# Kernel tuning notes

Hardware: AMD Instinct MI355X
Metric: run time of the kernel (lower is better)

## Reference

```python
import jax, jax.numpy as jnp
import numpy as np

WS = 8          # window_size
DISP = WS // 2  # cyclic shift displacement
HEADS = 12
HEAD_DIM = 32
SCALE = HEAD_DIM ** -0.5


def _rel_indices():
    # indices of (x, y) for x in range(WS) for y in range(WS)
    idx = np.stack(np.meshgrid(np.arange(WS), np.arange(WS), indexing='ij'), -1).reshape(-1, 2)
    return idx[None, :, :] - idx[:, None, :] + WS - 1  # (WS^2, WS^2, 2), values in [0, 2*WS-2]


def _masks():
    ninf = -np.inf
    # upper/lower mask: blocks attention across the vertical wrap boundary
    m_ul = np.zeros((WS * WS, WS * WS), np.float32)
    m_ul[-DISP * WS:, :-DISP * WS] = ninf
    m_ul[:-DISP * WS, -DISP * WS:] = ninf
    # left/right mask: blocks attention across the horizontal wrap boundary
    m4 = np.zeros((WS, WS, WS, WS), np.float32)  # (h1, w1, h2, w2)
    m4[:, -DISP:, :, :-DISP] = ninf
    m4[:, :-DISP, :, -DISP:] = ninf
    m_lr = m4.reshape(WS * WS, WS * WS)
    return jnp.asarray(m_ul), jnp.asarray(m_lr)


def setup_inputs() -> dict:
    key = jax.random.key(0)
    k1, k2, k3, k4, k5 = jax.random.split(key, 5)
    dim = HEADS * HEAD_DIM  # 384
    return {
        'x': jax.random.normal(k1, (16, 64, 64, dim), jnp.float32),
        'w_qkv': jax.random.normal(k2, (dim, 3 * dim), jnp.float32) * 0.02,
        'pos_embedding': jax.random.normal(k3, (2 * WS - 1, 2 * WS - 1), jnp.float32),
        'w_out': jax.random.normal(k4, (dim, dim), jnp.float32) * 0.02,
        'b_out': jax.random.normal(k5, (dim,), jnp.float32) * 0.02,
    }


def reference(x, w_qkv, pos_embedding, w_out, b_out):
    b, H, W, dim = x.shape
    nw_h, nw_w = H // WS, W // WS
    # cyclic shift
    x = jnp.roll(x, (-DISP, -DISP), axis=(1, 2))
    qkv = x @ w_qkv  # (b, H, W, 3*inner)

    def to_windows(t):
        # (b, H, W, inner) -> (b, heads, nw_h*nw_w, WS*WS, head_dim)
        t = t.reshape(b, nw_h, WS, nw_w, WS, HEADS, HEAD_DIM)
        return t.transpose(0, 5, 1, 3, 2, 4, 6).reshape(b, HEADS, nw_h * nw_w, WS * WS, HEAD_DIM)

    q, k, v = [to_windows(t) for t in jnp.split(qkv, 3, axis=-1)]
    dots = jnp.einsum('bhwid,bhwjd->bhwij', q, k) * SCALE

    rel = _rel_indices()
    dots = dots + pos_embedding[rel[..., 0], rel[..., 1]]  # relative position bias

    m_ul, m_lr = _masks()
    dots = dots.at[:, :, -nw_w:].add(m_ul)            # last row of windows
    dots = dots.at[:, :, nw_w - 1::nw_w].add(m_lr)    # last column of windows

    attn = jax.nn.softmax(dots, axis=-1)
    out = jnp.einsum('bhwij,bhwjd->bhwid', attn, v)
    # windows -> image layout
    out = out.reshape(b, HEADS, nw_h, nw_w, WS, WS, HEAD_DIM)
    out = out.transpose(0, 2, 4, 3, 5, 1, 6).reshape(b, H, W, HEADS * HEAD_DIM)
    out = out @ w_out + b_out
    # cyclic back shift
    return jnp.roll(out, (DISP, DISP), axis=(1, 2))
```

## Files before the change

kernel.cpp:

```cpp
#include <hip/hip_runtime.h>
#include <stdint.h>

#define HEADS 12
#define HD 32
#define DIM 384
#define NQKV 1152
#define NPIX 4096
#define NB 16

typedef __attribute__((ext_vector_type(8))) short bf16x8;
typedef __attribute__((ext_vector_type(4))) short bf16x4;
typedef __attribute__((ext_vector_type(4))) float f32x4;

__device__ __forceinline__ unsigned short f2bf(float f) {
  uint32_t u = __builtin_bit_cast(uint32_t, f);
  u += 0x7FFF + ((u >> 16) & 1);
  return (unsigned short)(u >> 16);
}

#define GL_LDS(gp, lp) __builtin_amdgcn_global_load_lds( \
    (const __attribute__((address_space(1))) void*)(gp),  \
    (__attribute__((address_space(3))) void*)(lp), 16, 0, 0)

__global__ void convert_all(const float* __restrict__ x,
                            const float* __restrict__ wqkv,
                            const float* __restrict__ wout,
                            const float* __restrict__ pos,
                            unsigned short* __restrict__ xb,
                            unsigned short* __restrict__ wqkvT,
                            unsigned short* __restrict__ woutT,
                            float* __restrict__ tab) {
  int bid = blockIdx.x;
  if (bid < 12288) {
    int i = bid * 256 + threadIdx.x;
    const float4* xp = (const float4*)x;
    float4 a = xp[2 * i], b2 = xp[2 * i + 1];
    union { bf16x8 v; unsigned short s[8]; } u;
    u.s[0] = f2bf(a.x);  u.s[1] = f2bf(a.y);
    u.s[2] = f2bf(a.z);  u.s[3] = f2bf(a.w);
    u.s[4] = f2bf(b2.x); u.s[5] = f2bf(b2.y);
    u.s[6] = f2bf(b2.z); u.s[7] = f2bf(b2.w);
    ((bf16x8*)xb)[i] = u.v;
  } else if (bid < 14016) {
    int tid = (bid - 12288) * 256 + threadIdx.x;
    if (tid < NQKV * DIM) {
      int n = tid / DIM, k = tid % DIM;
      wqkvT[tid] = f2bf(wqkv[(size_t)k * NQKV + n]);
    }
    if (tid < DIM * DIM) {
      int n = tid / DIM, k = tid % DIM;
      woutT[tid] = f2bf(wout[(size_t)k * DIM + n]);
    }
  } else {
    int tid = (bid - 14016) * 256 + threadIdx.x;
    int v = tid >> 12, rem = tid & 4095;
    int i = rem >> 6, j = rem & 63;
    int xi = i >> 3, yi = i & 7, xj = j >> 3, yj = j & 7;
    float val = pos[(xj - xi + 7) * 15 + (yj - yi + 7)];
    if ((v & 1) && ((i >= 32) != (j >= 32))) val = -1e30f;
    if ((v & 2) && ((yi >= 4) != (yj >= 4))) val = -1e30f;
    tab[tid] = val;
  }
}

__global__ __launch_bounds__(256, 4) void gemm_qkv(
    const unsigned short* __restrict__ xb,
    const unsigned short* __restrict__ wT,
    unsigned short* __restrict__ qkv)
{
  __shared__ unsigned short lA[128 * 64];
  __shared__ unsigned short lB[128 * 64];
  const int tid = threadIdx.x;
  const int wid = tid >> 6, lane = tid & 63;
  const int wr = wid >> 1, wc = wid & 1;
  const int lr = lane >> 4, lc = lane & 15;

  const int f = blockIdx.x;
  const int xcd = f & 7, idx = f >> 3;
  const int nt = idx % 9, mt = xcd * 64 + idx / 9;
  const int m0 = mt * 128, n0 = nt * 128;

  const int srow = wid * 32 + (lane >> 3);
  const int scol = ((lane & 7) ^ (lane >> 3)) * 8;
  const unsigned short* agp = xb + (size_t)(m0 + srow) * DIM + scol;
  const unsigned short* bgp = wT + (size_t)(n0 + srow) * DIM + scol;

  const f32x4 z4 = {0.f, 0.f, 0.f, 0.f};
  f32x4 acc[4][4];
#pragma unroll
  for (int i = 0; i < 4; i++)
#pragma unroll
    for (int j = 0; j < 4; j++) acc[i][j] = z4;

  auto stage = [&](int t) {
#pragma unroll
    for (int i = 0; i < 4; i++) {
      GL_LDS(agp + (size_t)(i * 8) * DIM + t * 64, &lA[(wid * 4 + i) * 512]);
      GL_LDS(bgp + (size_t)(i * 8) * DIM + t * 64, &lB[(wid * 4 + i) * 512]);
    }
  };
  auto compute = [&]() {
    const int sw = lc & 7;
#pragma unroll
    for (int kk = 0; kk < 2; kk++) {
      bf16x8 afr[4], bfr[4];
#pragma unroll
      for (int mi = 0; mi < 4; mi++)
        afr[mi] = *(const bf16x8*)&lA[(wr * 64 + mi * 16 + lc) * 64 + (((kk * 4 + lr) ^ sw) * 8)];
#pragma unroll
      for (int ni = 0; ni < 4; ni++)
        bfr[ni] = *(const bf16x8*)&lB[(wc * 64 + ni * 16 + lc) * 64 + (((kk * 4 + lr) ^ sw) * 8)];
#pragma unroll
      for (int mi = 0; mi < 4; mi++)
#pragma unroll
        for (int ni = 0; ni < 4; ni++)
          acc[mi][ni] = __builtin_amdgcn_mfma_f32_16x16x32_bf16(afr[mi], bfr[ni], acc[mi][ni], 0, 0, 0);
    }
  };

  for (int t = 0; t < 6; ++t) {
    stage(t);
    __syncthreads();
    compute();
    if (t < 5) __syncthreads();
  }

#pragma unroll
  for (int mi = 0; mi < 4; mi++) {
    int row = m0 + wr * 64 + mi * 16 + lr * 4;
#pragma unroll
    for (int reg = 0; reg < 4; reg++) {
      size_t rb = (size_t)(row + reg) * NQKV + n0 + wc * 64 + lc;
#pragma unroll
      for (int ni = 0; ni < 4; ni++)
        qkv[rb + ni * 16] = f2bf(acc[mi][ni][reg]);
    }
  }
}

__global__ __launch_bounds__(256) void attn_kernel(
    const unsigned short* __restrict__ qkv,
    const float* __restrict__ tab,
    unsigned short* __restrict__ Z)
{
  __shared__ unsigned short Vt[4][32 * 80];

  const int wid = threadIdx.x >> 6, lane = threadIdx.x & 63;
  const int lr = lane >> 4, lc = lane & 15;
  const int task = blockIdx.x * 4 + wid;
  const int win = task & 63;
  const int head = (task >> 6) % HEADS;
  const int b = task / (HEADS * 64);
  const int wh = win >> 3, ww = win & 7;
  const float* tv = tab + (((wh == 7) ? 1 : 0) + ((ww == 7) ? 2 : 0)) * 4096;

  auto pixof = [&](int t) {
    int hh = (wh * 8 + (t >> 3) + 4) & 63;
    int w2 = (ww * 8 + (t & 7) + 4) & 63;
    return hh * 64 + w2;
  };

  unsigned short* vt = &Vt[wid][0];
  bf16x8 qf[4], kf[4];
#pragma unroll
  for (int g = 0; g < 4; ++g) {
    int t = g * 16 + lc;
    const unsigned short* base =
        qkv + (size_t)(b * NPIX + pixof(t)) * NQKV + head * HD + lr * 8;
    qf[g] = *(const bf16x8*)(base);
    kf[g] = *(const bf16x8*)(base + DIM);
    union { bf16x8 v; unsigned short s[8]; } uv;
    uv.v = *(const bf16x8*)(base + 2 * DIM);
#pragma unroll
    for (int j = 0; j < 8; j++) {
      int row = lr * 8 + j;
      int addr = row * 80 + (((g * 2 + (lc >> 3)) ^ ((row >> 2) & 3)) << 3) + (lc & 7);
      vt[addr] = uv.s[j];
    }
  }

  const float SC = 0.17677669529663687f;
  const f32x4 z4 = {0.f, 0.f, 0.f, 0.f};
  uint32_t pf[4][2][4];
  const int srcA = (lc + 16 * (2 * (lr & 1))) << 2;
  const int srcB = srcA + 64;
  const bool hiSel = (lr >> 1) != 0;

#pragma unroll
  for (int bq = 0; bq < 4; bq++) {
    f32x4 tb[4];
#pragma unroll
    for (int a = 0; a < 4; a++)
      tb[a] = *(const f32x4*)&tv[(bq * 16 + lc) * 64 + a * 16 + lr * 4];
    f32x4 s[4];
#pragma unroll
    for (int a = 0; a < 4; a++)
      s[a] = __builtin_amdgcn_mfma_f32_16x16x32_bf16(kf[a], qf[bq], z4, 0, 0, 0);

    float m = -3.0e38f;
#pragma unroll
    for (int a = 0; a < 4; a++)
#pragma unroll
      for (int r = 0; r < 4; r++) {
        float val = s[a][r] * SC + tb[a][r];
        s[a][r] = val;
        m = fmaxf(m, val);
      }
    m = fmaxf(m, __shfl_xor(m, 16));
    m = fmaxf(m, __shfl_xor(m, 32));
    float sum = 0.f;
#pragma unroll
    for (int a = 0; a < 4; a++)
#pragma unroll
      for (int r = 0; r < 4; r++) {
        float p = exp2f((s[a][r] - m) * 1.44269504f);
        s[a][r] = p;
        sum += p;
      }
    sum += __shfl_xor(sum, 16);
    sum += __shfl_xor(sum, 32);
    float iv = 1.0f / sum;

    uint32_t pk[4][2];
#pragma unroll
    for (int a = 0; a < 4; a++)
#pragma unroll
      for (int w = 0; w < 2; w++) {
        float plo = s[a][2 * w] * iv, phi = s[a][2 * w + 1] * iv;
        uint32_t r;
        asm("v_cvt_pk_bf16_f32 %0, %1, %2" : "=v"(r) : "v"(plo), "v"(phi));
        pk[a][w] = r;
      }
#pragma unroll
    for (int kk = 0; kk < 2; kk++)
#pragma unroll
      for (int wp = 0; wp < 4; wp++) {
        int sa = (wp >> 1) ? srcB : srcA;
        uint32_t lo = (uint32_t)__builtin_amdgcn_ds_bpermute(sa, (int)pk[2 * kk][wp & 1]);
        uint32_t hi = (uint32_t)__builtin_amdgcn_ds_bpermute(sa, (int)pk[2 * kk + 1][wp & 1]);
        pf[bq][kk][wp] = hiSel ? hi : lo;
      }
  }

  asm volatile("s_waitcnt lgkmcnt(0)" ::: "memory");

  f32x4 oacc[4][2];
#pragma unroll
  for (int i = 0; i < 4; i++) { oacc[i][0] = z4; oacc[i][1] = z4; }

#pragma unroll
  for (int kk = 0; kk < 2; kk++) {
    bf16x8 vfr[2];
#pragma unroll
    for (int dt = 0; dt < 2; dt++) {
      int rowd = dt * 16 + lc;
      int addr = rowd * 80 + ((((kk * 4 + lr) ^ (lc >> 2)) & 7) << 3);
      vfr[dt] = *(const bf16x8*)&vt[addr];
    }
#pragma unroll
    for (int mi = 0; mi < 4; mi++) {
      union { uint32_t u[4]; bf16x8 v; } pu;
      pu.u[0] = pf[mi][kk][0]; pu.u[1] = pf[mi][kk][1];
      pu.u[2] = pf[mi][kk][2]; pu.u[3] = pf[mi][kk][3];
#pragma unroll
      for (int dt = 0; dt < 2; dt++)
        oacc[mi][dt] = __builtin_amdgcn_mfma_f32_16x16x32_bf16(pu.v, vfr[dt], oacc[mi][dt], 0, 0, 0);
    }
  }

#pragma unroll
  for (int mi = 0; mi < 4; mi++) {
#pragma unroll
    for (int reg = 0; reg < 4; reg++) {
      int i = mi * 16 + lr * 4 + reg;
      size_t zb = ((size_t)b * NPIX + pixof(i)) * DIM + head * HD;
#pragma unroll
      for (int dt = 0; dt < 2; dt++)
        Z[zb + dt * 16 + lc] = f2bf(oacc[mi][dt][reg]);
    }
  }
}

__global__ __launch_bounds__(256, 4) void gemm_out(
    const unsigned short* __restrict__ Zb,
    const unsigned short* __restrict__ wT,
    const float* __restrict__ bout,
    float* __restrict__ out)
{
  __shared__ unsigned short lA[128 * 64];
  __shared__ unsigned short lB[128 * 64];
  const int tid = threadIdx.x;
  const int wid = tid >> 6, lane = tid & 63;
  const int wr = wid >> 1, wc = wid & 1;
  const int lr = lane >> 4, lc = lane & 15;

  const int f = blockIdx.x;
  const int xcd = f & 7, idx = f >> 3;
  const int nt = idx % 3, mt = xcd * 64 + idx / 3;
  const int m0 = mt * 128, n0 = nt * 128;

  const int srow = wid * 32 + (lane >> 3);
  const int scol = ((lane & 7) ^ (lane >> 3)) * 8;
  const unsigned short* agp = Zb + (size_t)(m0 + srow) * DIM + scol;
  const unsigned short* bgp = wT + (size_t)(n0 + srow) * DIM + scol;

  const f32x4 z4 = {0.f, 0.f, 0.f, 0.f};
  f32x4 acc[4][4];
#pragma unroll
  for (int i = 0; i < 4; i++)
#pragma unroll
    for (int j = 0; j < 4; j++) acc[i][j] = z4;

  auto stage = [&](int t) {
#pragma unroll
    for (int i = 0; i < 4; i++) {
      GL_LDS(agp + (size_t)(i * 8) * DIM + t * 64, &lA[(wid * 4 + i) * 512]);
      GL_LDS(bgp + (size_t)(i * 8) * DIM + t * 64, &lB[(wid * 4 + i) * 512]);
    }
  };
  auto compute = [&]() {
    const int sw = lc & 7;
#pragma unroll
    for (int kk = 0; kk < 2; kk++) {
      bf16x8 afr[4], bfr[4];
#pragma unroll
      for (int mi = 0; mi < 4; mi++)
        afr[mi] = *(const bf16x8*)&lA[(wr * 64 + mi * 16 + lc) * 64 + (((kk * 4 + lr) ^ sw) * 8)];
#pragma unroll
      for (int ni = 0; ni < 4; ni++)
        bfr[ni] = *(const bf16x8*)&lB[(wc * 64 + ni * 16 + lc) * 64 + (((kk * 4 + lr) ^ sw) * 8)];
#pragma unroll
      for (int mi = 0; mi < 4; mi++)
#pragma unroll
        for (int ni = 0; ni < 4; ni++)
          acc[mi][ni] = __builtin_amdgcn_mfma_f32_16x16x32_bf16(afr[mi], bfr[ni], acc[mi][ni], 0, 0, 0);
    }
  };

  for (int t = 0; t < 6; ++t) {
    stage(t);
    __syncthreads();
    compute();
    if (t < 5) __syncthreads();
  }

  float bo[4];
#pragma unroll
  for (int ni = 0; ni < 4; ni++) bo[ni] = bout[n0 + wc * 64 + ni * 16 + lc];

#pragma unroll
  for (int mi = 0; mi < 4; mi++) {
    int row = m0 + wr * 64 + mi * 16 + lr * 4;
#pragma unroll
    for (int reg = 0; reg < 4; reg++) {
      size_t rb = (size_t)(row + reg) * DIM + n0 + wc * 64 + lc;
#pragma unroll
      for (int ni = 0; ni < 4; ni++)
        out[rb + ni * 16] = acc[mi][ni][reg] + bo[ni];
    }
  }
}

extern "C" void kernel_launch(void* const* d_in, const int* in_sizes, int n_in,
                              void* d_out, int out_size, void* d_ws, size_t ws_size,
                              hipStream_t stream) {
  const float* x    = (const float*)d_in[0];
  const float* wqkv = (const float*)d_in[1];
  const float* pos  = (const float*)d_in[2];
  const float* wout = (const float*)d_in[3];
  const float* bout = (const float*)d_in[4];
  float* out = (float*)d_out;

  char* ws = (char*)d_ws;
  unsigned short* wqkvT = (unsigned short*)ws;
  unsigned short* woutT = (unsigned short*)(ws + 884736);
  unsigned short* qkv   = (unsigned short*)(ws + 1179648);
  unsigned short* xb    = (unsigned short*)(ws + 1179648 + 150994944);
  unsigned short* Zb    = xb;
  float* tab = out;

  convert_all<<<14080, 256, 0, stream>>>(x, wqkv, wout, pos, xb, wqkvT, woutT, tab);
  gemm_qkv<<<4608, 256, 0, stream>>>(xb, wqkvT, qkv);
  attn_kernel<<<3072, 256, 0, stream>>>(qkv, tab, Zb);
  gemm_out<<<1536, 256, 0, stream>>>(Zb, woutT, bout, out);
}
```

Before: 179.0 us.

## Fuse x conversion into per-window QKV projection reading fp32 directly

Removes the separate pass that converts x to bf16 and replaces the tiled QKV GEMM with a per-window kernel. Each block loads one shifted 8x8 window of fp32 x, converts it into swizzled LDS, and computes Q, K and V for three heads per wave using MFMA, reading weights straight from global memory. This drops one full write and read of the bf16 activation tensor and a kernel launch. In exchange, weight fragments are re-read from global/L2 for every window, there is no LDS staging of B, and occupancy drops because of the large LDS footprint and launch bound of 2.

```diff
diff --git a/kernel.cpp b/kernel.cpp
--- a/kernel.cpp
+++ b/kernel.cpp
@@ -9,7 +9,6 @@
 #define NB 16
 
 typedef __attribute__((ext_vector_type(8))) short bf16x8;
-typedef __attribute__((ext_vector_type(4))) short bf16x4;
 typedef __attribute__((ext_vector_type(4))) float f32x4;
 
 __device__ __forceinline__ unsigned short f2bf(float f) {
@@ -22,27 +21,17 @@
     (const __attribute__((address_space(1))) void*)(gp),  \
     (__attribute__((address_space(3))) void*)(lp), 16, 0, 0)
 
-__global__ void convert_all(const float* __restrict__ x,
-                            const float* __restrict__ wqkv,
-                            const float* __restrict__ wout,
-                            const float* __restrict__ pos,
-                            unsigned short* __restrict__ xb,
-                            unsigned short* __restrict__ wqkvT,
-                            unsigned short* __restrict__ woutT,
-                            float* __restrict__ tab) {
+#define MFMA32 __builtin_amdgcn_mfma_f32_16x16x32_bf16
+
+__global__ void convert_w(const float* __restrict__ wqkv,
+                          const float* __restrict__ wout,
+                          const float* __restrict__ pos,
+                          unsigned short* __restrict__ wqkvT,
+                          unsigned short* __restrict__ woutT,
+                          float* __restrict__ tab) {
   int bid = blockIdx.x;
-  if (bid < 12288) {
-    int i = bid * 256 + threadIdx.x;
-    const float4* xp = (const float4*)x;
-    float4 a = xp[2 * i], b2 = xp[2 * i + 1];
-    union { bf16x8 v; unsigned short s[8]; } u;
-    u.s[0] = f2bf(a.x);  u.s[1] = f2bf(a.y);
-    u.s[2] = f2bf(a.z);  u.s[3] = f2bf(a.w);
-    u.s[4] = f2bf(b2.x); u.s[5] = f2bf(b2.y);
-    u.s[6] = f2bf(b2.z); u.s[7] = f2bf(b2.w);
-    ((bf16x8*)xb)[i] = u.v;
-  } else if (bid < 14016) {
-    int tid = (bid - 12288) * 256 + threadIdx.x;
+  if (bid < 1728) {
+    int tid = bid * 256 + threadIdx.x;
     if (tid < NQKV * DIM) {
       int n = tid / DIM, k = tid % DIM;
       wqkvT[tid] = f2bf(wqkv[(size_t)k * NQKV + n]);
@@ -52,7 +41,7 @@
       woutT[tid] = f2bf(wout[(size_t)k * DIM + n]);
     }
   } else {
-    int tid = (bid - 14016) * 256 + threadIdx.x;
+    int tid = (bid - 1728) * 256 + threadIdx.x;
     int v = tid >> 12, rem = tid & 4095;
     int i = rem >> 6, j = rem & 63;
     int xi = i >> 3, yi = i & 7, xj = j >> 3, yj = j & 7;
@@ -63,78 +52,97 @@
   }
 }
 
-__global__ __launch_bounds__(256, 4) void gemm_qkv(
-    const unsigned short* __restrict__ xb,
+__global__ __launch_bounds__(256, 2) void qkv_direct(
+    const float* __restrict__ x,
     const unsigned short* __restrict__ wT,
     unsigned short* __restrict__ qkv)
 {
-  __shared__ unsigned short lA[128 * 64];
-  __shared__ unsigned short lB[128 * 64];
+  __shared__ unsigned short Xs[64 * DIM];
+
   const int tid = threadIdx.x;
   const int wid = tid >> 6, lane = tid & 63;
-  const int wr = wid >> 1, wc = wid & 1;
   const int lr = lane >> 4, lc = lane & 15;
-
-  const int f = blockIdx.x;
-  const int xcd = f & 7, idx = f >> 3;
-  const int nt = idx % 9, mt = xcd * 64 + idx / 9;
-  const int m0 = mt * 128, n0 = nt * 128;
-
-  const int srow = wid * 32 + (lane >> 3);
-  const int scol = ((lane & 7) ^ (lane >> 3)) * 8;
-  const unsigned short* agp = xb + (size_t)(m0 + srow) * DIM + scol;
-  const unsigned short* bgp = wT + (size_t)(n0 + srow) * DIM + scol;
+  const int task = blockIdx.x;
+  const int win = task & 63, b = task >> 6;
+  const int wh = win >> 3, ww = win & 7;
+
+  auto pixof = [&](int t) {
+    int hh = (wh * 8 + (t >> 3) + 4) & 63;
+    int w2 = (ww * 8 + (t & 7) + 4) & 63;
+    return hh * 64 + w2;
+  };
+
+  {
+    const int pix = tid >> 2;
+    const float* xrow = x + (size_t)(b * NPIX + pixof(pix)) * DIM;
+    unsigned short* xr = &Xs[pix * DIM];
+    const int sw = pix & 7;
+#pragma unroll
+    for (int pass = 0; pass < 12; ++pass) {
+      const int g = (tid & 3) + pass * 4;
+      float4 a0 = *(const float4*)(xrow + g * 8);
+      float4 a1 = *(const float4*)(xrow + g * 8 + 4);
+      union { unsigned short s[8]; bf16x8 v; } u;
+      u.s[0] = f2bf(a0.x); u.s[1] = f2bf(a0.y);
+      u.s[2] = f2bf(a0.z); u.s[3] = f2bf(a0.w);
+      u.s[4] = f2bf(a1.x); u.s[5] = f2bf(a1.y);
+      u.s[6] = f2bf(a1.z); u.s[7] = f2bf(a1.w);
+      *(bf16x8*)&xr[(g ^ sw) * 8] = u.v;
+    }
+  }
+  __syncthreads();
 
   const f32x4 z4 = {0.f, 0.f, 0.f, 0.f};
-  f32x4 acc[4][4];
-#pragma unroll
-  for (int i = 0; i < 4; i++)
-#pragma unroll
-    for (int j = 0; j < 4; j++) acc[i][j] = z4;
-
-  auto stage = [&](int t) {
-#pragma unroll
-    for (int i = 0; i < 4; i++) {
-      GL_LDS(agp + (size_t)(i * 8) * DIM + t * 64, &lA[(wid * 4 + i) * 512]);
-      GL_LDS(bgp + (size_t)(i * 8) * DIM + t * 64, &lB[(wid * 4 + i) * 512]);
-    }
-  };
-  auto compute = [&]() {
-    const int sw = lc & 7;
-#pragma unroll
-    for (int kk = 0; kk < 2; kk++) {
-      bf16x8 afr[4], bfr[4];
-#pragma unroll
-      for (int mi = 0; mi < 4; mi++)
-        afr[mi] = *(const bf16x8*)&lA[(wr * 64 + mi * 16 + lc) * 64 + (((kk * 4 + lr) ^ sw) * 8)];
-#pragma unroll
-      for (int ni = 0; ni < 4; ni++)
-        bfr[ni] = *(const bf16x8*)&lB[(wc * 64 + ni * 16 + lc) * 64 + (((kk * 4 + lr) ^ sw) * 8)];
-#pragma unroll
-      for (int mi = 0; mi < 4; mi++)
-#pragma unroll
-        for (int ni = 0; ni < 4; ni++)
-          acc[mi][ni] = __builtin_amdgcn_mfma_f32_16x16x32_bf16(afr[mi], bfr[ni], acc[mi][ni], 0, 0, 0);
-    }
-  };
-
-  for (int t = 0; t < 6; ++t) {
-    stage(t);
-    __syncthreads();
-    compute();
-    if (t < 5) __syncthreads();
-  }
-
-#pragma unroll
-  for (int mi = 0; mi < 4; mi++) {
-    int row = m0 + wr * 64 + mi * 16 + lr * 4;
-#pragma unroll
-    for (int reg = 0; reg < 4; reg++) {
-      size_t rb = (size_t)(row + reg) * NQKV + n0 + wc * 64 + lc;
-#pragma unroll
-      for (int ni = 0; ni < 4; ni++)
-        qkv[rb + ni * 16] = f2bf(acc[mi][ni][reg]);
-    }
+  const int xsw = lc & 7;
+
+  for (int hi = 0; hi < 3; ++hi) {
+    const int h = wid * 3 + hi;
+    const unsigned short* wbase = wT + (size_t)(h * 32 + lc) * DIM + lr * 8;
+
+    f32x4 qa[2][4], ka[2][4], vt[2][4];
+#pragma unroll
+    for (int dt = 0; dt < 2; dt++)
+#pragma unroll
+      for (int jt = 0; jt < 4; jt++) { qa[dt][jt] = z4; ka[dt][jt] = z4; vt[dt][jt] = z4; }
+
+    for (int ks = 0; ks < 12; ++ks) {
+      bf16x8 xf[4];
+#pragma unroll
+      for (int jt = 0; jt < 4; ++jt)
+        xf[jt] = *(const bf16x8*)&Xs[(jt * 16 + lc) * DIM + (((ks * 4 + lr) ^ xsw) * 8)];
+      bf16x8 wf[3][2];
+#pragma unroll
+      for (int mat = 0; mat < 3; ++mat)
+#pragma unroll
+        for (int dt = 0; dt < 2; ++dt)
+          wf[mat][dt] = *(const bf16x8*)(wbase + (size_t)mat * 147456 + dt * 6144 + ks * 32);
+#pragma unroll
+      for (int dt = 0; dt < 2; ++dt)
+#pragma unroll
+        for (int jt = 0; jt < 4; ++jt) {
+          qa[dt][jt] = MFMA32(wf[0][dt], xf[jt], qa[dt][jt], 0, 0, 0);
+          ka[dt][jt] = MFMA32(wf[1][dt], xf[jt], ka[dt][jt], 0, 0, 0);
+          vt[dt][jt] = MFMA32(wf[2][dt], xf[jt], vt[dt][jt], 0, 0, 0);
+        }
+    }
+
+#pragma unroll
+    for (int dt = 0; dt < 2; ++dt)
+#pragma unroll
+      for (int t4 = 0; t4 < 4; ++t4) {
+        size_t base = ((size_t)b * NPIX + pixof(t4 * 16 + lc)) * NQKV
+                      + h * HD + dt * 16 + lr * 4;
+        union { unsigned short s[4]; uint2 v; } uq, uk, uv;
+#pragma unroll
+        for (int r = 0; r < 4; ++r) {
+          uq.s[r] = f2bf(qa[dt][t4][r]);
+          uk.s[r] = f2bf(ka[dt][t4][r]);
+          uv.s[r] = f2bf(vt[dt][t4][r]);
+        }
+        *(uint2*)&qkv[base] = uq.v;
+        *(uint2*)&qkv[base + DIM] = uk.v;
+        *(uint2*)&qkv[base + 2 * DIM] = uv.v;
+      }
   }
 }
 
@@ -195,7 +203,7 @@
     f32x4 s[4];
 #pragma unroll
     for (int a = 0; a < 4; a++)
-      s[a] = __builtin_amdgcn_mfma_f32_16x16x32_bf16(kf[a], qf[bq], z4, 0, 0, 0);
+      s[a] = MFMA32(kf[a], qf[bq], z4, 0, 0, 0);
 
     float m = -3.0e38f;
 #pragma unroll
@@ -264,7 +272,7 @@
       pu.u[2] = pf[mi][kk][2]; pu.u[3] = pf[mi][kk][3];
 #pragma unroll
       for (int dt = 0; dt < 2; dt++)
-        oacc[mi][dt] = __builtin_amdgcn_mfma_f32_16x16x32_bf16(pu.v, vfr[dt], oacc[mi][dt], 0, 0, 0);
+        oacc[mi][dt] = MFMA32(pu.v, vfr[dt], oacc[mi][dt], 0, 0, 0);
     }
   }
 
@@ -333,7 +341,7 @@
       for (int mi = 0; mi < 4; mi++)
 #pragma unroll
         for (int ni = 0; ni < 4; ni++)
-          acc[mi][ni] = __builtin_amdgcn_mfma_f32_16x16x32_bf16(afr[mi], bfr[ni], acc[mi][ni], 0, 0, 0);
+          acc[mi][ni] = MFMA32(afr[mi], bfr[ni], acc[mi][ni], 0, 0, 0);
     }
   };
 
@@ -375,12 +383,11 @@
   unsigned short* wqkvT = (unsigned short*)ws;
   unsigned short* woutT = (unsigned short*)(ws + 884736);
   unsigned short* qkv   = (unsigned short*)(ws + 1179648);
-  unsigned short* xb    = (unsigned short*)(ws + 1179648 + 150994944);
-  unsigned short* Zb    = xb;
+  unsigned short* Zb    = (unsigned short*)(ws + 1179648 + 150994944);
   float* tab = out;
 
-  convert_all<<<14080, 256, 0, stream>>>(x, wqkv, wout, pos, xb, wqkvT, woutT, tab);
-  gemm_qkv<<<4608, 256, 0, stream>>>(xb, wqkvT, qkv);
+  convert_w<<<1792, 256, 0, stream>>>(wqkv, wout, pos, wqkvT, woutT, tab);
+  qkv_direct<<<1024, 256, 0, stream>>>(x, wqkvT, qkv);
   attn_kernel<<<3072, 256, 0, stream>>>(qkv, tab, Zb);
   gemm_out<<<1536, 256, 0, stream>>>(Zb, woutT, bout, out);
 }
```

Result: slower. 339.8 us (+89.9%).

## Fuse fp32-to-bf16 conversion of x into the QKV GEMM's LDS tile load

Applied to the files above, without the earlier changes.

Drops the separate pass that converts the 100MB fp32 activation x to bf16. The QKV GEMM now stages fp32 rows of x straight into LDS through a new XOR-swizzled layout and converts them to bf16 with packed converts while building MFMA fragments. This removes a full read and write of x plus one round trip through the intermediate buffer. In exchange, the A tile doubles in LDS size, occupancy is lowered to 3 blocks, and x is loaded once per N tile (9 times) at fp32 width.

```diff
diff --git a/kernel.cpp b/kernel.cpp
--- a/kernel.cpp
+++ b/kernel.cpp
@@ -9,7 +9,6 @@
 #define NB 16
 
 typedef __attribute__((ext_vector_type(8))) short bf16x8;
-typedef __attribute__((ext_vector_type(4))) short bf16x4;
 typedef __attribute__((ext_vector_type(4))) float f32x4;
 
 __device__ __forceinline__ unsigned short f2bf(float f) {
@@ -18,31 +17,27 @@
   return (unsigned short)(u >> 16);
 }
 
+__device__ __forceinline__ uint32_t cvtpk(float lo, float hi) {
+  uint32_t r;
+  asm("v_cvt_pk_bf16_f32 %0, %1, %2" : "=v"(r) : "v"(lo), "v"(hi));
+  return r;
+}
+
 #define GL_LDS(gp, lp) __builtin_amdgcn_global_load_lds( \
     (const __attribute__((address_space(1))) void*)(gp),  \
     (__attribute__((address_space(3))) void*)(lp), 16, 0, 0)
 
-__global__ void convert_all(const float* __restrict__ x,
-                            const float* __restrict__ wqkv,
-                            const float* __restrict__ wout,
-                            const float* __restrict__ pos,
-                            unsigned short* __restrict__ xb,
-                            unsigned short* __restrict__ wqkvT,
-                            unsigned short* __restrict__ woutT,
-                            float* __restrict__ tab) {
+#define MFMA32 __builtin_amdgcn_mfma_f32_16x16x32_bf16
+
+__global__ void convert_w(const float* __restrict__ wqkv,
+                          const float* __restrict__ wout,
+                          const float* __restrict__ pos,
+                          unsigned short* __restrict__ wqkvT,
+                          unsigned short* __restrict__ woutT,
+                          float* __restrict__ tab) {
   int bid = blockIdx.x;
-  if (bid < 12288) {
-    int i = bid * 256 + threadIdx.x;
-    const float4* xp = (const float4*)x;
-    float4 a = xp[2 * i], b2 = xp[2 * i + 1];
-    union { bf16x8 v; unsigned short s[8]; } u;
-    u.s[0] = f2bf(a.x);  u.s[1] = f2bf(a.y);
-    u.s[2] = f2bf(a.z);  u.s[3] = f2bf(a.w);
-    u.s[4] = f2bf(b2.x); u.s[5] = f2bf(b2.y);
-    u.s[6] = f2bf(b2.z); u.s[7] = f2bf(b2.w);
-    ((bf16x8*)xb)[i] = u.v;
-  } else if (bid < 14016) {
-    int tid = (bid - 12288) * 256 + threadIdx.x;
+  if (bid < 1728) {
+    int tid = bid * 256 + threadIdx.x;
     if (tid < NQKV * DIM) {
       int n = tid / DIM, k = tid % DIM;
       wqkvT[tid] = f2bf(wqkv[(size_t)k * NQKV + n]);
@@ -52,7 +47,7 @@
       woutT[tid] = f2bf(wout[(size_t)k * DIM + n]);
     }
   } else {
-    int tid = (bid - 14016) * 256 + threadIdx.x;
+    int tid = (bid - 1728) * 256 + threadIdx.x;
     int v = tid >> 12, rem = tid & 4095;
     int i = rem >> 6, j = rem & 63;
     int xi = i >> 3, yi = i & 7, xj = j >> 3, yj = j & 7;
@@ -63,12 +58,12 @@
   }
 }
 
-__global__ __launch_bounds__(256, 4) void gemm_qkv(
-    const unsigned short* __restrict__ xb,
+__global__ __launch_bounds__(256, 3) void gemm_qkv(
+    const float* __restrict__ x,
     const unsigned short* __restrict__ wT,
     unsigned short* __restrict__ qkv)
 {
-  __shared__ unsigned short lA[128 * 64];
+  __shared__ float lAf[128 * 64];
   __shared__ unsigned short lB[128 * 64];
   const int tid = threadIdx.x;
   const int wid = tid >> 6, lane = tid & 63;
@@ -80,10 +75,13 @@
   const int nt = idx % 9, mt = xcd * 64 + idx / 9;
   const int m0 = mt * 128, n0 = nt * 128;
 
-  const int srow = wid * 32 + (lane >> 3);
-  const int scol = ((lane & 7) ^ (lane >> 3)) * 8;
-  const unsigned short* agp = xb + (size_t)(m0 + srow) * DIM + scol;
-  const unsigned short* bgp = wT + (size_t)(n0 + srow) * DIM + scol;
+  const int sArow = wid * 4 + (lane >> 4);
+  const int sAcol = ((lane & 15) ^ sArow) * 4;
+  const float* agp = x + (size_t)(m0 + sArow) * DIM + sAcol;
+
+  const int sBrow = wid * 32 + (lane >> 3);
+  const int sBcol = ((lane & 7) ^ (lane >> 3)) * 8;
+  const unsigned short* bgp = wT + (size_t)(n0 + sBrow) * DIM + sBcol;
 
   const f32x4 z4 = {0.f, 0.f, 0.f, 0.f};
   f32x4 acc[4][4];
@@ -94,27 +92,38 @@
 
   auto stage = [&](int t) {
 #pragma unroll
-    for (int i = 0; i < 4; i++) {
-      GL_LDS(agp + (size_t)(i * 8) * DIM + t * 64, &lA[(wid * 4 + i) * 512]);
+    for (int i = 0; i < 8; i++)
+      GL_LDS(agp + (size_t)(i * 16) * DIM + t * 64, &lAf[i * 1024 + wid * 256]);
+#pragma unroll
+    for (int i = 0; i < 4; i++)
       GL_LDS(bgp + (size_t)(i * 8) * DIM + t * 64, &lB[(wid * 4 + i) * 512]);
-    }
   };
   auto compute = [&]() {
-    const int sw = lc & 7;
+    const int swb = lc & 7;
 #pragma unroll
     for (int kk = 0; kk < 2; kk++) {
       bf16x8 afr[4], bfr[4];
 #pragma unroll
+      for (int mi = 0; mi < 4; mi++) {
+        const int r = wr * 64 + mi * 16 + lc;
+        const int g0 = kk * 8 + lr * 2;
+        float4 a0 = *(const float4*)&lAf[r * 64 + ((g0 ^ lc) * 4)];
+        float4 a1 = *(const float4*)&lAf[r * 64 + (((g0 + 1) ^ lc) * 4)];
+        union { uint32_t u[4]; bf16x8 v; } up;
+        up.u[0] = cvtpk(a0.x, a0.y);
+        up.u[1] = cvtpk(a0.z, a0.w);
+        up.u[2] = cvtpk(a1.x, a1.y);
+        up.u[3] = cvtpk(a1.z, a1.w);
+        afr[mi] = up.v;
+      }
+#pragma unroll
+      for (int ni = 0; ni < 4; ni++)
+        bfr[ni] = *(const bf16x8*)&lB[(wc * 64 + ni * 16 + lc) * 64 + (((kk * 4 + lr) ^ swb) * 8)];
+#pragma unroll
       for (int mi = 0; mi < 4; mi++)
-        afr[mi] = *(const bf16x8*)&lA[(wr * 64 + mi * 16 + lc) * 64 + (((kk * 4 + lr) ^ sw) * 8)];
-#pragma unroll
-      for (int ni = 0; ni < 4; ni++)
-        bfr[ni] = *(const bf16x8*)&lB[(wc * 64 + ni * 16 + lc) * 64 + (((kk * 4 + lr) ^ sw) * 8)];
-#pragma unroll
-      for (int mi = 0; mi < 4; mi++)
 #pragma unroll
         for (int ni = 0; ni < 4; ni++)
-          acc[mi][ni] = __builtin_amdgcn_mfma_f32_16x16x32_bf16(afr[mi], bfr[ni], acc[mi][ni], 0, 0, 0);
+          acc[mi][ni] = MFMA32(afr[mi], bfr[ni], acc[mi][ni], 0, 0, 0);
     }
   };
 
@@ -195,7 +204,7 @@
     f32x4 s[4];
 #pragma unroll
     for (int a = 0; a < 4; a++)
-      s[a] = __builtin_amdgcn_mfma_f32_16x16x32_bf16(kf[a], qf[bq], z4, 0, 0, 0);
+      s[a] = MFMA32(kf[a], qf[bq], z4, 0, 0, 0);
 
     float m = -3.0e38f;
 #pragma unroll
@@ -225,12 +234,8 @@
 #pragma unroll
     for (int a = 0; a < 4; a++)
 #pragma unroll
-      for (int w = 0; w < 2; w++) {
-        float plo = s[a][2 * w] * iv, phi = s[a][2 * w + 1] * iv;
-        uint32_t r;
-        asm("v_cvt_pk_bf16_f32 %0, %1, %2" : "=v"(r) : "v"(plo), "v"(phi));
-        pk[a][w] = r;
-      }
+      for (int w = 0; w < 2; w++)
+        pk[a][w] = cvtpk(s[a][2 * w] * iv, s[a][2 * w + 1] * iv);
 #pragma unroll
     for (int kk = 0; kk < 2; kk++)
 #pragma unroll
@@ -264,7 +269,7 @@
       pu.u[2] = pf[mi][kk][2]; pu.u[3] = pf[mi][kk][3];
 #pragma unroll
       for (int dt = 0; dt < 2; dt++)
-        oacc[mi][dt] = __builtin_amdgcn_mfma_f32_16x16x32_bf16(pu.v, vfr[dt], oacc[mi][dt], 0, 0, 0);
+        oacc[mi][dt] = MFMA32(pu.v, vfr[dt], oacc[mi][dt], 0, 0, 0);
     }
   }
 
@@ -333,7 +338,7 @@
       for (int mi = 0; mi < 4; mi++)
 #pragma unroll
         for (int ni = 0; ni < 4; ni++)
-          acc[mi][ni] = __builtin_amdgcn_mfma_f32_16x16x32_bf16(afr[mi], bfr[ni], acc[mi][ni], 0, 0, 0);
+          acc[mi][ni] = MFMA32(afr[mi], bfr[ni], acc[mi][ni], 0, 0, 0);
     }
   };
 
@@ -375,12 +380,11 @@
   unsigned short* wqkvT = (unsigned short*)ws;
   unsigned short* woutT = (unsigned short*)(ws + 884736);
   unsigned short* qkv   = (unsigned short*)(ws + 1179648);
-  unsigned short* xb    = (unsigned short*)(ws + 1179648 + 150994944);
-  unsigned short* Zb    = xb;
+  unsigned short* Zb    = (unsigned short*)(ws + 1179648 + 150994944);
   float* tab = out;
 
-  convert_all<<<14080, 256, 0, stream>>>(x, wqkv, wout, pos, xb, wqkvT, woutT, tab);
-  gemm_qkv<<<4608, 256, 0, stream>>>(xb, wqkvT, qkv);
+  convert_w<<<1792, 256, 0, stream>>>(wqkv, wout, pos, wqkvT, woutT, tab);
+  gemm_qkv<<<4608, 256, 0, stream>>>(x, wqkvT, qkv);
   attn_kernel<<<3072, 256, 0, stream>>>(qkv, tab, Zb);
   gemm_out<<<1536, 256, 0, stream>>>(Zb, woutT, bout, out);
 }
```

Result: slower. 213.0 us (+19.0%).
